# Optimization experiments

Measured on AMD Instinct MI355X. Metric: run time of the kernel, lower is better.

Reference implementation:

```python
import jax, jax.numpy as jnp
import numpy as np

SPLINE_ORDER = 3
TOP_K = 2
NUM_EXPERTS = 8


def _gram_basis(x, beta_w):
    # x: (B, C, H, W) post-tanh. Returns (B, C*(S+1), H, W).
    P0 = jnp.ones_like(x)
    P1 = x
    ps = [P0, P1]
    for i in range(2, SPLINE_ORDER + 1):
        n, m = i - 1, i
        # beta(n, m) = (m+n)*(m-n)*n^2 / (m^2/(4n^2-1)) * beta_weights[n]
        beta = (m + n) * (m - n) * (n ** 2) * (4.0 * n ** 2 - 1.0) / (m ** 2) * beta_w[n]
        P2 = x * ps[-1] - beta * ps[-2]
        ps.append(P2)
    return jnp.concatenate(ps, axis=1)


def _expert(x, poly_w, beta_w):
    # tanh -> Gram polynomial basis -> SiLU -> conv2d (padding=1, stride=1)
    g = jax.nn.silu(_gram_basis(jnp.tanh(x), beta_w))
    return jax.lax.conv_general_dilated(
        g, poly_w[0], window_strides=(1, 1), padding=[(1, 1), (1, 1)],
        dimension_numbers=('NCHW', 'OIHW', 'NCHW'))


def _cv_squared(v):
    # torch.var is unbiased (ddof=1)
    return jnp.var(v, ddof=1) / (jnp.mean(v) ** 2 + 1e-10)


def reference(x, w_gate, poly_weights, beta_weights):
    B = x.shape[0]
    # gating input: global average pool -> (B, C)
    gate_x = jnp.mean(x, axis=(2, 3))
    probs = jax.nn.softmax(gate_x @ w_gate, axis=1)  # softmax BEFORE topk, as in source
    top_vals, top_idx = jax.lax.top_k(probs, TOP_K + 1)
    tk_vals = top_vals[:, :TOP_K]
    tk_idx = top_idx[:, :TOP_K]
    tk_gates = tk_vals / (jnp.sum(tk_vals, axis=1, keepdims=True) + 1e-6)
    gates = jnp.zeros_like(probs).at[jnp.arange(B)[:, None], tk_idx].set(tk_gates)
    importance = gates.sum(axis=0)
    load = jnp.sum(gates > 0, axis=0).astype(jnp.float32)  # eval-mode load
    loss = (_cv_squared(importance) + _cv_squared(load)) * 0.01
    # All experts share parameters (ModuleList([experts]*num_experts)), so
    # sum_e gates[b,e] * expert_e(x[b]) == gates.sum(1)[b] * expert(x[b]).
    y = _expert(x, poly_weights, beta_weights) * jnp.sum(gates, axis=1)[:, None, None, None]
    return y, loss


def setup_inputs() -> dict:
    key = jax.random.key(0)
    k1, k2, k3, k4 = jax.random.split(key, 4)
    x = jax.random.normal(k1, (16, 32, 192, 192), dtype=jnp.float32)
    w_gate = jax.random.normal(k2, (32, NUM_EXPERTS), dtype=jnp.float32) * 0.1
    poly_weights = jax.random.normal(k3, (1, 32, 32 * (SPLINE_ORDER + 1), 3, 3), dtype=jnp.float32) * 0.05
    beta_weights = jax.random.normal(k4, (SPLINE_ORDER + 1,), dtype=jnp.float32) * 0.01
    return {"x": x, "w_gate": w_gate, "poly_weights": poly_weights, "beta_weights": beta_weights}
```

## Files before the change

### kernel.cpp

```cpp
#include <hip/hip_runtime.h>

typedef unsigned short u16;
typedef unsigned int u32;
typedef __attribute__((ext_vector_type(8))) short bf16x8;
typedef __attribute__((ext_vector_type(4))) float f32x4;

static constexpr int B = 16, C = 32, H = 192, W = 192;
static constexpr int HW = H * W;
static constexpr int E = 8;
static constexpr int CO = 32;
static constexpr int NB = 96;
static constexpr long long NTOT = (long long)B * C * HW;
static constexpr float SILU1 = 0.7310585786300049f;

static constexpr size_t GP_OFF  = (size_t)NTOT * 2;
static constexpr size_t SCL_OFF = GP_OFF + (size_t)B * C * NB * 4;
static constexpr size_t SK_OFF  = SCL_OFF + 128;
static constexpr size_t SS_OFF  = SK_OFF + 288 * 4;
static constexpr size_t WF_OFF  = SS_OFF + 128;

__device__ inline u32 cvt_pk_bf16(float lo, float hi) {
    u32 r;
    asm("v_cvt_pk_bf16_f32 %0, %1, %2" : "=v"(r) : "v"(lo), "v"(hi));
    return r;
}
__device__ inline u16 f2b(float f) {
    u32 u = __float_as_uint(f);
    return (u16)((u + 0x7fffu + ((u >> 16) & 1u)) >> 16);
}
__device__ inline float silu_fast(float z) {
    return z * __builtin_amdgcn_rcpf(1.0f + __expf(-z));
}
__device__ inline float tanh_fast(float z) {
    float e = __expf(2.0f * z);
    return 1.0f - 2.0f * __builtin_amdgcn_rcpf(e + 1.0f);
}

__global__ __launch_bounds__(256) void stage1_prep(const float* __restrict__ x,
                                                   const float* __restrict__ pw,
                                                   u16* __restrict__ t_out,
                                                   float* __restrict__ gpart,
                                                   float* __restrict__ Sk,
                                                   float* __restrict__ Ssum,
                                                   u16* __restrict__ wfrag) {
    __shared__ float sg[2][4][16];
    __shared__ float sred[9][32][8];
    __shared__ float sks[288];
    const int blk = blockIdx.x, tid = threadIdx.x;
    if (blk < B * NB) {
        const int b = blk / NB, band = blk - (blk / NB) * NB;
        const int cp = tid & 15, part = tid >> 4;
        const size_t pbase = (size_t)b * HW + (size_t)(band * 2) * W;
        const float4* xa = (const float4*)(x + (size_t)(b * C + 2 * cp) * HW
                                             + (size_t)(band * 2) * W);
        const float4* xb = (const float4*)(x + (size_t)(b * C + 2 * cp + 1) * HW
                                             + (size_t)(band * 2) * W);
        u32* tw = (u32*)t_out;
        float s0 = 0.0f, s1 = 0.0f;
        #pragma unroll
        for (int k = 0; k < 6; ++k) {
            const int j = k * 16 + part;
            float4 a = xa[j], c = xb[j];
            s0 += (a.x + a.y) + (a.z + a.w);
            s1 += (c.x + c.y) + (c.z + c.w);
            u32 r0 = cvt_pk_bf16(tanh_fast(a.x), tanh_fast(c.x));
            u32 r1 = cvt_pk_bf16(tanh_fast(a.y), tanh_fast(c.y));
            u32 r2 = cvt_pk_bf16(tanh_fast(a.z), tanh_fast(c.z));
            u32 r3 = cvt_pk_bf16(tanh_fast(a.w), tanh_fast(c.w));
            u32* dst = tw + (pbase + (size_t)j * 4) * 16 + cp;
            dst[0] = r0; dst[16] = r1; dst[32] = r2; dst[48] = r3;
        }
        s0 += __shfl_down(s0, 32); s0 += __shfl_down(s0, 16);
        s1 += __shfl_down(s1, 32); s1 += __shfl_down(s1, 16);
        if ((part & 3) == 0) { sg[0][tid >> 6][cp] = s0; sg[1][tid >> 6][cp] = s1; }
        __syncthreads();
        if (tid < 32) {
            const int cpp = tid >> 1, o = tid & 1;
            gpart[(size_t)(b * C + tid) * NB + band] =
                (sg[o][0][cpp] + sg[o][1][cpp]) + (sg[o][2][cpp] + sg[o][3][cpp]);
        }
        return;
    }
    if (blk < B * NB + 108) {
        int j = (blk - B * NB) * 256 + tid;
        int e = j & 7, lane = (j >> 3) & 63, rest = j >> 9;
        int half = rest & 1, pt = rest >> 1;
        int p = pt / 9, tap = pt - p * 9;
        int co = half * 16 + (lane & 15);
        int ci = 32 + p * 32 + (lane >> 4) * 8 + e;
        wfrag[j] = f2b(pw[(size_t)co * 1152 + ci * 9 + tap]);
        return;
    }
    {
        const int co = tid & 31, sub = tid >> 5;
        #pragma unroll
        for (int k = 0; k < 9; ++k) {
            float s = 0.0f;
            #pragma unroll
            for (int i = 0; i < 4; ++i)
                s += pw[(size_t)co * 1152 + (sub * 4 + i) * 9 + k];
            sred[k][co][sub] = s;
        }
        __syncthreads();
        for (int j = tid; j < 288; j += 256) {
            int k = j >> 5, c = j & 31;
            float s = 0.0f;
            #pragma unroll
            for (int u = 0; u < 8; ++u) s += sred[k][c][u];
            sks[j] = s; Sk[j] = s;
        }
        __syncthreads();
        if (tid < 32) {
            float s = 0.0f;
            #pragma unroll
            for (int k = 0; k < 9; ++k) s += sks[k * 32 + tid];
            Ssum[tid] = s;
        }
    }
}

__global__ __launch_bounds__(512) void gate_k(const float* __restrict__ gpart,
                                              const float* __restrict__ wg,
                                              float* __restrict__ scl,
                                              float* __restrict__ out) {
    __shared__ float gx[B][C];
    __shared__ float lg[B][E];
    __shared__ float gt[B][E];
    const int tid = threadIdx.x;
    {
        const float4* gp = (const float4*)(gpart + (size_t)tid * NB);
        float s = 0.0f;
        #pragma unroll
        for (int k = 0; k < NB / 4; ++k) { float4 v = gp[k]; s += (v.x + v.y) + (v.z + v.w); }
        gx[tid >> 5][tid & 31] = s * (1.0f / HW);
    }
    __syncthreads();
    if (tid < B * E) {
        const int gb = tid >> 3, ge = tid & 7;
        float s = 0.0f;
        #pragma unroll
        for (int c = 0; c < C; ++c) s += gx[gb][c] * wg[c * E + ge];
        lg[gb][ge] = s;
    }
    __syncthreads();
    if (tid < B) {
        float p[E];
        float m = lg[tid][0];
        #pragma unroll
        for (int e = 1; e < E; ++e) m = fmaxf(m, lg[tid][e]);
        float sum = 0.0f;
        #pragma unroll
        for (int e = 0; e < E; ++e) { p[e] = __expf(lg[tid][e] - m); sum += p[e]; }
        float inv = 1.0f / sum;
        #pragma unroll
        for (int e = 0; e < E; ++e) p[e] *= inv;
        int i0 = 0; float v0g = p[0];
        #pragma unroll
        for (int e = 1; e < E; ++e) if (p[e] > v0g) { v0g = p[e]; i0 = e; }
        int i1 = -1; float v1g = -1.0f;
        #pragma unroll
        for (int e = 0; e < E; ++e) { if (e == i0) continue; if (p[e] > v1g) { v1g = p[e]; i1 = e; } }
        const float denom = v0g + v1g + 1e-6f;
        #pragma unroll
        for (int e = 0; e < E; ++e) gt[tid][e] = 0.0f;
        gt[tid][i0] = v0g / denom; gt[tid][i1] = v1g / denom;
        scl[tid] = gt[tid][i0] + gt[tid][i1];
    }
    __syncthreads();
    if (tid == 0) {
        float imp[E], ld[E];
        #pragma unroll
        for (int e = 0; e < E; ++e) { imp[e] = 0.0f; ld[e] = 0.0f; }
        for (int bb = 0; bb < B; ++bb)
            #pragma unroll
            for (int e = 0; e < E; ++e) {
                float g = gt[bb][e];
                imp[e] += g;
                if (g > 0.0f) ld[e] += 1.0f;
            }
        float mi = 0.0f, mld = 0.0f;
        #pragma unroll
        for (int e = 0; e < E; ++e) { mi += imp[e]; mld += ld[e]; }
        mi *= (1.0f / E); mld *= (1.0f / E);
        float vi = 0.0f, vl = 0.0f;
        #pragma unroll
        for (int e = 0; e < E; ++e) {
            float di = imp[e] - mi, dl = ld[e] - mld;
            vi += di * di; vl += dl * dl;
        }
        vi *= (1.0f / (E - 1)); vl *= (1.0f / (E - 1));
        out[NTOT] = (vi / (mi * mi + 1e-10f) + vl / (mld * mld + 1e-10f)) * 0.01f;
    }
}

static constexpr int GSTR = 40;

__global__ __launch_bounds__(256, 3) void conv_mfma(const u16* __restrict__ t_ws,
                                                 const u16* __restrict__ wfrag,
                                                 const float* __restrict__ beta_w,
                                                 const float* __restrict__ scl_ws,
                                                 const float* __restrict__ Sk,
                                                 const float* __restrict__ Ssum,
                                                 float* __restrict__ out) {
    __shared__ __align__(16) u16 gtile[2][324 * GSTR];

    const int b = blockIdx.z;
    const int gx0 = blockIdx.x << 4, gy0 = blockIdx.y << 4;
    const int tid = threadIdx.x;
    const int w = tid >> 6, lane = tid & 63, q = lane >> 4, ml = lane & 15;
    const float beta2 = 2.25f * beta_w[1];
    const float beta23 = beta2 + (300.0f / 9.0f) * beta_w[2];

    const int p0 = tid;
    int extra = -1;
    if ((tid & 3) == 0) extra = tid >> 2;
    else if ((tid & 63) == 1) extra = 64 + (tid >> 6);
    const int p1 = (extra >= 0) ? 256 + extra : -1;

    u32 pk0[16], pk1[16];
    bool v0, v1 = false;
    {
        int py = p0 / 18, px = p0 - py * 18;
        int gy = gy0 + py - 1, gx = gx0 + px - 1;
        v0 = (unsigned)gy < (unsigned)H && (unsigned)gx < (unsigned)W;
        if (v0) {
            const uint4* tp = (const uint4*)(t_ws + (((size_t)b * HW + (size_t)gy * W + gx) << 5));
            *(uint4*)&pk0[0]  = tp[0];
            *(uint4*)&pk0[4]  = tp[1];
            *(uint4*)&pk0[8]  = tp[2];
            *(uint4*)&pk0[12] = tp[3];
        } else {
            #pragma unroll
            for (int cc = 0; cc < 16; ++cc) pk0[cc] = 0u;
        }
        if (p1 >= 0) {
            int py1 = p1 / 18, px1 = p1 - py1 * 18;
            int gy1 = gy0 + py1 - 1, gx1 = gx0 + px1 - 1;
            v1 = (unsigned)gy1 < (unsigned)H && (unsigned)gx1 < (unsigned)W;
            if (v1) {
                const uint4* tp = (const uint4*)(t_ws + (((size_t)b * HW + (size_t)gy1 * W + gx1) << 5));
                *(uint4*)&pk1[0]  = tp[0];
                *(uint4*)&pk1[4]  = tp[1];
                *(uint4*)&pk1[8]  = tp[2];
                *(uint4*)&pk1[12] = tp[3];
            }
        }
        if (!v1) {
            #pragma unroll
            for (int cc = 0; cc < 16; ++cc) pk1[cc] = 0u;
        }
    }

    const float sc = scl_ws[b];

#define BQUAD(P, BUF, SLOT, QI)                                                 \
    do {                                                                        \
        if (!(SLOT) || p1 >= 0) {                                               \
            const bool vv = (SLOT) ? v1 : v0;                                   \
            const u32* pk = (SLOT) ? pk1 : pk0;                                 \
            const int pix = (SLOT) ? p1 : p0;                                   \
            u32 rq[4];                                                          \
            if (vv) {                                                           \
                _Pragma("unroll")                                               \
                for (int i = 0; i < 4; ++i) {                                   \
                    const int cc = (QI) * 4 + i;                                \
                    float tl = __uint_as_float(pk[cc] << 16);                   \
                    float th = __uint_as_float(pk[cc] & 0xffff0000u);           \
                    float ul, uh;                                               \
                    if ((P) == 0) { ul = tl; uh = th; }                         \
                    else if ((P) == 1) { ul = fmaf(tl, tl, -beta2); uh = fmaf(th, th, -beta2); } \
                    else { ul = tl * fmaf(tl, tl, -beta23); uh = th * fmaf(th, th, -beta23); } \
                    rq[i] = cvt_pk_bf16(silu_fast(ul), silu_fast(uh));          \
                }                                                               \
            } else { rq[0] = 0u; rq[1] = 0u; rq[2] = 0u; rq[3] = 0u; }          \
            *(uint4*)&gtile[BUF][pix * GSTR + (QI) * 8] = *(const uint4*)rq;    \
        }                                                                       \
    } while (0)

    f32x4 acc[4][2];
    #pragma unroll
    for (int a = 0; a < 4; ++a) {
        acc[a][0] = (f32x4){0.0f, 0.0f, 0.0f, 0.0f};
        acc[a][1] = (f32x4){0.0f, 0.0f, 0.0f, 0.0f};
    }

#define MFMA_DX(P, BUF, DX, ...)                                                \
    do {                                                                        \
        const u16* wf = wfrag + (size_t)(P) * 9216;                             \
        bf16x8 bfr[3][2];                                                       \
        _Pragma("unroll")                                                       \
        for (int dyi = 0; dyi < 3; ++dyi) {                                     \
            const int tap = dyi * 3 + (DX);                                     \
            bfr[dyi][0] = *(const bf16x8*)(wf + ((size_t)(tap * 2 + 0) * 64 + lane) * 8); \
            bfr[dyi][1] = *(const bf16x8*)(wf + ((size_t)(tap * 2 + 1) * 64 + lane) * 8); \
        }                                                                       \
        bf16x8 af6[6];                                                          \
        _Pragma("unroll")                                                       \
        for (int rl = 0; rl < 6; ++rl)                                          \
            af6[rl] = *(const bf16x8*)                                          \
                &gtile[BUF][(((w << 2) + rl) * 18 + ml + (DX)) * GSTR + (q << 3)]; \
        __VA_ARGS__;                                                            \
        _Pragma("unroll")                                                       \
        for (int rl = 0; rl < 6; ++rl) {                                        \
            _Pragma("unroll")                                                   \
            for (int dyi = 0; dyi < 3; ++dyi) {                                 \
                const int a = rl - dyi;                                         \
                if (a >= 0 && a < 4) {                                          \
                    acc[a][0] = __builtin_amdgcn_mfma_f32_16x16x32_bf16(af6[rl], bfr[dyi][0], acc[a][0], 0, 0, 0); \
                    acc[a][1] = __builtin_amdgcn_mfma_f32_16x16x32_bf16(af6[rl], bfr[dyi][1], acc[a][1], 0, 0, 0); \
                }                                                               \
            }                                                                   \
        }                                                                       \
    } while (0)

    BQUAD(0, 0, 0, 0); BQUAD(0, 0, 0, 1); BQUAD(0, 0, 0, 2); BQUAD(0, 0, 0, 3);
    BQUAD(0, 0, 1, 0); BQUAD(0, 0, 1, 1); BQUAD(0, 0, 1, 2); BQUAD(0, 0, 1, 3);
    __syncthreads();
    MFMA_DX(0, 0, 0, BQUAD(1, 1, 0, 0); BQUAD(1, 1, 0, 1); BQUAD(1, 1, 0, 2));
    MFMA_DX(0, 0, 1, BQUAD(1, 1, 0, 3); BQUAD(1, 1, 1, 0); BQUAD(1, 1, 1, 1));
    MFMA_DX(0, 0, 2, BQUAD(1, 1, 1, 2); BQUAD(1, 1, 1, 3));
    __syncthreads();
    MFMA_DX(1, 1, 0, BQUAD(2, 0, 0, 0); BQUAD(2, 0, 0, 1); BQUAD(2, 0, 0, 2));
    MFMA_DX(1, 1, 1, BQUAD(2, 0, 0, 3); BQUAD(2, 0, 1, 0); BQUAD(2, 0, 1, 1));
    MFMA_DX(1, 1, 2, BQUAD(2, 0, 1, 2); BQUAD(2, 0, 1, 3));
    __syncthreads();
    MFMA_DX(2, 0, 0, (void)0);
    MFMA_DX(2, 0, 1, (void)0);
    MFMA_DX(2, 0, 2, (void)0);

#undef BQUAD
#undef MFMA_DX

    const bool interior = (blockIdx.x > 0) && (blockIdx.x < 11) &&
                          (blockIdx.y > 0) && (blockIdx.y < 11);
    #pragma unroll
    for (int half = 0; half < 2; ++half) {
        const int co = half * 16 + ml;
        const float bfull = SILU1 * Ssum[co];
        #pragma unroll
        for (int a = 0; a < 4; ++a) {
            const int y = gy0 + (w << 2) + a;
            float ov[4];
            #pragma unroll
            for (int r = 0; r < 4; ++r) {
                float bias = bfull;
                if (!interior) {
                    const int xg = gx0 + (q << 2) + r;
                    bias = 0.0f;
                    #pragma unroll
                    for (int k = 0; k < 9; ++k) {
                        int yy = y + k / 3 - 1, xx = xg + k % 3 - 1;
                        if ((unsigned)yy < (unsigned)H && (unsigned)xx < (unsigned)W)
                            bias += Sk[k * 32 + co];
                    }
                    bias *= SILU1;
                }
                ov[r] = (acc[a][half][r] + bias) * sc;
            }
            *(float4*)&out[((size_t)(b * CO + co) * H + y) * W + gx0 + (q << 2)] = *(float4*)ov;
        }
    }
}

extern "C" void kernel_launch(void* const* d_in, const int* in_sizes, int n_in,
                              void* d_out, int out_size, void* d_ws, size_t ws_size,
                              hipStream_t stream) {
    const float* x  = (const float*)d_in[0];
    const float* wg = (const float*)d_in[1];
    const float* pw = (const float*)d_in[2];
    const float* bw = (const float*)d_in[3];
    float* out = (float*)d_out;
    char* ws = (char*)d_ws;
    u16*   t_ws  = (u16*)ws;
    float* gpart = (float*)(ws + GP_OFF);
    float* scl   = (float*)(ws + SCL_OFF);
    float* Sk    = (float*)(ws + SK_OFF);
    float* Ssum  = (float*)(ws + SS_OFF);
    u16*   wfrag = (u16*)(ws + WF_OFF);

    stage1_prep<<<dim3(B * NB + 109), 256, 0, stream>>>(x, pw, t_ws, gpart, Sk, Ssum, wfrag);
    gate_k<<<dim3(1), 512, 0, stream>>>(gpart, wg, scl, out);
    conv_mfma<<<dim3(12, 12, B), 256, 0, stream>>>(t_ws, wfrag, bw, scl, Sk, Ssum, out);
}
```

Measured before the change: 242.2 us.

## Fuse gating into prep kernel, stage tanh via LDS, single-buffer conv tile

The separate gate kernel is folded into stage1_prep: the last band block, found with an atomic counter, computes the softmax, top-k gates and loss. Stage1 now transposes the bf16 tanh values through an LDS tile and writes coalesced 64-byte pixel rows instead of strided 32-bit stores. The conv kernel drops its double-buffered basis tile in favour of one buffer with sequential basis/MFMA phases, and raises launch bounds to 6 blocks per CU for more occupancy. This gives up the overlap of basis computation with MFMA and adds a memset and atomic serialization.

```diff
diff --git a/kernel.cpp b/kernel.cpp
--- a/kernel.cpp
+++ b/kernel.cpp
@@ -18,6 +18,7 @@
 static constexpr size_t SK_OFF  = SCL_OFF + 128;
 static constexpr size_t SS_OFF  = SK_OFF + 288 * 4;
 static constexpr size_t WF_OFF  = SS_OFF + 128;
+static constexpr size_t CNT_OFF = WF_OFF + 27648 * 2;
 
 __device__ inline u32 cvt_pk_bf16(float lo, float hi) {
     u32 r;
@@ -36,48 +37,133 @@
     return 1.0f - 2.0f * __builtin_amdgcn_rcpf(e + 1.0f);
 }
 
+static constexpr int TBS = 40;
+
 __global__ __launch_bounds__(256) void stage1_prep(const float* __restrict__ x,
                                                    const float* __restrict__ pw,
+                                                   const float* __restrict__ wg,
                                                    u16* __restrict__ t_out,
                                                    float* __restrict__ gpart,
                                                    float* __restrict__ Sk,
                                                    float* __restrict__ Ssum,
-                                                   u16* __restrict__ wfrag) {
-    __shared__ float sg[2][4][16];
-    __shared__ float sred[9][32][8];
-    __shared__ float sks[288];
+                                                   u16* __restrict__ wfrag,
+                                                   float* __restrict__ scl,
+                                                   u32* __restrict__ cnt,
+                                                   float* __restrict__ out) {
+    __shared__ __align__(16) char smem[384 * TBS * 2];
+    __shared__ u32 lastflag;
     const int blk = blockIdx.x, tid = threadIdx.x;
     if (blk < B * NB) {
         const int b = blk / NB, band = blk - (blk / NB) * NB;
-        const int cp = tid & 15, part = tid >> 4;
+        const int c = tid >> 3, s = tid & 7;
+        u16* tb = (u16*)smem;
+        const float4* xp = (const float4*)(x + (size_t)(b * C + c) * HW
+                                             + (size_t)(band * 2) * W);
+        float gsum = 0.0f;
+        #pragma unroll
+        for (int it = 0; it < 12; ++it) {
+            const int j = it * 8 + s;
+            float4 v = xp[j];
+            gsum += (v.x + v.y) + (v.z + v.w);
+            const int px = j * 4;
+            tb[(px + 0) * TBS + c] = f2b(tanh_fast(v.x));
+            tb[(px + 1) * TBS + c] = f2b(tanh_fast(v.y));
+            tb[(px + 2) * TBS + c] = f2b(tanh_fast(v.z));
+            tb[(px + 3) * TBS + c] = f2b(tanh_fast(v.w));
+        }
+        gsum += __shfl_down(gsum, 4, 8);
+        gsum += __shfl_down(gsum, 2, 8);
+        gsum += __shfl_down(gsum, 1, 8);
+        if (s == 0) gpart[(size_t)(b * C + c) * NB + band] = gsum;
+        __syncthreads();
         const size_t pbase = (size_t)b * HW + (size_t)(band * 2) * W;
-        const float4* xa = (const float4*)(x + (size_t)(b * C + 2 * cp) * HW
-                                             + (size_t)(band * 2) * W);
-        const float4* xb = (const float4*)(x + (size_t)(b * C + 2 * cp + 1) * HW
-                                             + (size_t)(band * 2) * W);
-        u32* tw = (u32*)t_out;
-        float s0 = 0.0f, s1 = 0.0f;
-        #pragma unroll
-        for (int k = 0; k < 6; ++k) {
-            const int j = k * 16 + part;
-            float4 a = xa[j], c = xb[j];
-            s0 += (a.x + a.y) + (a.z + a.w);
-            s1 += (c.x + c.y) + (c.z + c.w);
-            u32 r0 = cvt_pk_bf16(tanh_fast(a.x), tanh_fast(c.x));
-            u32 r1 = cvt_pk_bf16(tanh_fast(a.y), tanh_fast(c.y));
-            u32 r2 = cvt_pk_bf16(tanh_fast(a.z), tanh_fast(c.z));
-            u32 r3 = cvt_pk_bf16(tanh_fast(a.w), tanh_fast(c.w));
-            u32* dst = tw + (pbase + (size_t)j * 4) * 16 + cp;
-            dst[0] = r0; dst[16] = r1; dst[32] = r2; dst[48] = r3;
-        }
-        s0 += __shfl_down(s0, 32); s0 += __shfl_down(s0, 16);
-        s1 += __shfl_down(s1, 32); s1 += __shfl_down(s1, 16);
-        if ((part & 3) == 0) { sg[0][tid >> 6][cp] = s0; sg[1][tid >> 6][cp] = s1; }
-        __syncthreads();
-        if (tid < 32) {
-            const int cpp = tid >> 1, o = tid & 1;
-            gpart[(size_t)(b * C + tid) * NB + band] =
-                (sg[o][0][cpp] + sg[o][1][cpp]) + (sg[o][2][cpp] + sg[o][3][cpp]);
+        uint4* tw = (uint4*)t_out;
+        {
+            const uint4* row = (const uint4*)(tb + tid * TBS);
+            uint4* dst = tw + (pbase + tid) * 4;
+            dst[0] = row[0]; dst[1] = row[1]; dst[2] = row[2]; dst[3] = row[3];
+        }
+        if (tid < 128) {
+            const int p = 256 + tid;
+            const uint4* row = (const uint4*)(tb + p * TBS);
+            uint4* dst = tw + (pbase + p) * 4;
+            dst[0] = row[0]; dst[1] = row[1]; dst[2] = row[2]; dst[3] = row[3];
+        }
+        __threadfence();
+        __syncthreads();
+        if (tid == 0) {
+            u32 tk = atomicAdd(cnt, 1u);
+            __threadfence();
+            lastflag = (tk == (u32)(B * NB - 1)) ? 1u : 0u;
+        }
+        __syncthreads();
+        if (!lastflag) return;
+        float* gxs = (float*)smem;
+        float* lgs = gxs + 512;
+        float* gts = lgs + 128;
+        for (int r = tid; r < B * C; r += 256) {
+            const float4* gp = (const float4*)(gpart + (size_t)r * NB);
+            float ss = 0.0f;
+            #pragma unroll
+            for (int k = 0; k < NB / 4; ++k) { float4 v = gp[k]; ss += (v.x + v.y) + (v.z + v.w); }
+            gxs[r] = ss * (1.0f / HW);
+        }
+        __syncthreads();
+        if (tid < B * E) {
+            const int gb = tid >> 3, ge = tid & 7;
+            float ssum = 0.0f;
+            #pragma unroll
+            for (int cc = 0; cc < C; ++cc) ssum += gxs[gb * 32 + cc] * wg[cc * E + ge];
+            lgs[tid] = ssum;
+        }
+        __syncthreads();
+        if (tid < B) {
+            float p[E];
+            float m = lgs[tid * E];
+            #pragma unroll
+            for (int e = 1; e < E; ++e) m = fmaxf(m, lgs[tid * E + e]);
+            float sum = 0.0f;
+            #pragma unroll
+            for (int e = 0; e < E; ++e) { p[e] = __expf(lgs[tid * E + e] - m); sum += p[e]; }
+            float inv = 1.0f / sum;
+            #pragma unroll
+            for (int e = 0; e < E; ++e) p[e] *= inv;
+            int i0 = 0; float v0g = p[0];
+            #pragma unroll
+            for (int e = 1; e < E; ++e) if (p[e] > v0g) { v0g = p[e]; i0 = e; }
+            int i1 = -1; float v1g = -1.0f;
+            #pragma unroll
+            for (int e = 0; e < E; ++e) { if (e == i0) continue; if (p[e] > v1g) { v1g = p[e]; i1 = e; } }
+            const float denom = v0g + v1g + 1e-6f;
+            #pragma unroll
+            for (int e = 0; e < E; ++e) gts[tid * E + e] = 0.0f;
+            gts[tid * E + i0] = v0g / denom; gts[tid * E + i1] = v1g / denom;
+            scl[tid] = gts[tid * E + i0] + gts[tid * E + i1];
+        }
+        __syncthreads();
+        if (tid == 0) {
+            float imp[E], ld[E];
+            #pragma unroll
+            for (int e = 0; e < E; ++e) { imp[e] = 0.0f; ld[e] = 0.0f; }
+            for (int bb = 0; bb < B; ++bb)
+                #pragma unroll
+                for (int e = 0; e < E; ++e) {
+                    float g = gts[bb * E + e];
+                    imp[e] += g;
+                    if (g > 0.0f) ld[e] += 1.0f;
+                }
+            float mi = 0.0f, mld = 0.0f;
+            #pragma unroll
+            for (int e = 0; e < E; ++e) { mi += imp[e]; mld += ld[e]; }
+            mi *= (1.0f / E); mld *= (1.0f / E);
+            float vi = 0.0f, vl = 0.0f;
+            #pragma unroll
+            for (int e = 0; e < E; ++e) {
+                float di = imp[e] - mi, dl = ld[e] - mld;
+                vi += di * di; vl += dl * dl;
+            }
+            vi *= (1.0f / (E - 1)); vl *= (1.0f / (E - 1));
+            out[NTOT] = (vi / (mi * mi + 1e-10f) + vl / (mld * mld + 1e-10f)) * 0.01f;
         }
         return;
     }
@@ -92,6 +178,8 @@
         return;
     }
     {
+        float* sred = (float*)smem;
+        float* sks  = (float*)(smem + 9216);
         const int co = tid & 31, sub = tid >> 5;
         #pragma unroll
         for (int k = 0; k < 9; ++k) {
@@ -99,14 +187,13 @@
             #pragma unroll
             for (int i = 0; i < 4; ++i)
                 s += pw[(size_t)co * 1152 + (sub * 4 + i) * 9 + k];
-            sred[k][co][sub] = s;
+            sred[(k * 32 + co) * 8 + sub] = s;
         }
         __syncthreads();
         for (int j = tid; j < 288; j += 256) {
-            int k = j >> 5, c = j & 31;
             float s = 0.0f;
             #pragma unroll
-            for (int u = 0; u < 8; ++u) s += sred[k][c][u];
+            for (int u = 0; u < 8; ++u) s += sred[j * 8 + u];
             sks[j] = s; Sk[j] = s;
         }
         __syncthreads();
@@ -119,90 +206,16 @@
     }
 }
 
-__global__ __launch_bounds__(512) void gate_k(const float* __restrict__ gpart,
-                                              const float* __restrict__ wg,
-                                              float* __restrict__ scl,
-                                              float* __restrict__ out) {
-    __shared__ float gx[B][C];
-    __shared__ float lg[B][E];
-    __shared__ float gt[B][E];
-    const int tid = threadIdx.x;
-    {
-        const float4* gp = (const float4*)(gpart + (size_t)tid * NB);
-        float s = 0.0f;
-        #pragma unroll
-        for (int k = 0; k < NB / 4; ++k) { float4 v = gp[k]; s += (v.x + v.y) + (v.z + v.w); }
-        gx[tid >> 5][tid & 31] = s * (1.0f / HW);
-    }
-    __syncthreads();
-    if (tid < B * E) {
-        const int gb = tid >> 3, ge = tid & 7;
-        float s = 0.0f;
-        #pragma unroll
-        for (int c = 0; c < C; ++c) s += gx[gb][c] * wg[c * E + ge];
-        lg[gb][ge] = s;
-    }
-    __syncthreads();
-    if (tid < B) {
-        float p[E];
-        float m = lg[tid][0];
-        #pragma unroll
-        for (int e = 1; e < E; ++e) m = fmaxf(m, lg[tid][e]);
-        float sum = 0.0f;
-        #pragma unroll
-        for (int e = 0; e < E; ++e) { p[e] = __expf(lg[tid][e] - m); sum += p[e]; }
-        float inv = 1.0f / sum;
-        #pragma unroll
-        for (int e = 0; e < E; ++e) p[e] *= inv;
-        int i0 = 0; float v0g = p[0];
-        #pragma unroll
-        for (int e = 1; e < E; ++e) if (p[e] > v0g) { v0g = p[e]; i0 = e; }
-        int i1 = -1; float v1g = -1.0f;
-        #pragma unroll
-        for (int e = 0; e < E; ++e) { if (e == i0) continue; if (p[e] > v1g) { v1g = p[e]; i1 = e; } }
-        const float denom = v0g + v1g + 1e-6f;
-        #pragma unroll
-        for (int e = 0; e < E; ++e) gt[tid][e] = 0.0f;
-        gt[tid][i0] = v0g / denom; gt[tid][i1] = v1g / denom;
-        scl[tid] = gt[tid][i0] + gt[tid][i1];
-    }
-    __syncthreads();
-    if (tid == 0) {
-        float imp[E], ld[E];
-        #pragma unroll
-        for (int e = 0; e < E; ++e) { imp[e] = 0.0f; ld[e] = 0.0f; }
-        for (int bb = 0; bb < B; ++bb)
-            #pragma unroll
-            for (int e = 0; e < E; ++e) {
-                float g = gt[bb][e];
-                imp[e] += g;
-                if (g > 0.0f) ld[e] += 1.0f;
-            }
-        float mi = 0.0f, mld = 0.0f;
-        #pragma unroll
-        for (int e = 0; e < E; ++e) { mi += imp[e]; mld += ld[e]; }
-        mi *= (1.0f / E); mld *= (1.0f / E);
-        float vi = 0.0f, vl = 0.0f;
-        #pragma unroll
-        for (int e = 0; e < E; ++e) {
-            float di = imp[e] - mi, dl = ld[e] - mld;
-            vi += di * di; vl += dl * dl;
-        }
-        vi *= (1.0f / (E - 1)); vl *= (1.0f / (E - 1));
-        out[NTOT] = (vi / (mi * mi + 1e-10f) + vl / (mld * mld + 1e-10f)) * 0.01f;
-    }
-}
-
 static constexpr int GSTR = 40;
 
-__global__ __launch_bounds__(256, 3) void conv_mfma(const u16* __restrict__ t_ws,
+__global__ __launch_bounds__(256, 6) void conv_mfma(const u16* __restrict__ t_ws,
                                                  const u16* __restrict__ wfrag,
                                                  const float* __restrict__ beta_w,
                                                  const float* __restrict__ scl_ws,
                                                  const float* __restrict__ Sk,
                                                  const float* __restrict__ Ssum,
                                                  float* __restrict__ out) {
-    __shared__ __align__(16) u16 gtile[2][324 * GSTR];
+    __shared__ __align__(16) u16 gtile[324 * GSTR];
 
     const int b = blockIdx.z;
     const int gx0 = blockIdx.x << 4, gy0 = blockIdx.y << 4;
@@ -253,27 +266,35 @@
 
     const float sc = scl_ws[b];
 
-#define BQUAD(P, BUF, SLOT, QI)                                                 \
+#define BASIS(P)                                                                \
     do {                                                                        \
-        if (!(SLOT) || p1 >= 0) {                                               \
-            const bool vv = (SLOT) ? v1 : v0;                                   \
-            const u32* pk = (SLOT) ? pk1 : pk0;                                 \
-            const int pix = (SLOT) ? p1 : p0;                                   \
-            u32 rq[4];                                                          \
+        _Pragma("unroll")                                                       \
+        for (int slot = 0; slot < 2; ++slot) {                                  \
+            const int pix = slot ? p1 : p0;                                     \
+            if (slot && p1 < 0) continue;                                       \
+            const bool vv = slot ? v1 : v0;                                     \
+            const u32* pk = slot ? pk1 : pk0;                                   \
+            u32 r[16];                                                          \
             if (vv) {                                                           \
                 _Pragma("unroll")                                               \
-                for (int i = 0; i < 4; ++i) {                                   \
-                    const int cc = (QI) * 4 + i;                                \
+                for (int cc = 0; cc < 16; ++cc) {                               \
                     float tl = __uint_as_float(pk[cc] << 16);                   \
                     float th = __uint_as_float(pk[cc] & 0xffff0000u);           \
                     float ul, uh;                                               \
                     if ((P) == 0) { ul = tl; uh = th; }                         \
                     else if ((P) == 1) { ul = fmaf(tl, tl, -beta2); uh = fmaf(th, th, -beta2); } \
                     else { ul = tl * fmaf(tl, tl, -beta23); uh = th * fmaf(th, th, -beta23); } \
-                    rq[i] = cvt_pk_bf16(silu_fast(ul), silu_fast(uh));          \
+                    r[cc] = cvt_pk_bf16(silu_fast(ul), silu_fast(uh));          \
                 }                                                               \
-            } else { rq[0] = 0u; rq[1] = 0u; rq[2] = 0u; rq[3] = 0u; }          \
-            *(uint4*)&gtile[BUF][pix * GSTR + (QI) * 8] = *(const uint4*)rq;    \
+            } else {                                                            \
+                _Pragma("unroll")                                               \
+                for (int cc = 0; cc < 16; ++cc) r[cc] = 0u;                     \
+            }                                                                   \
+            uint4* dst = (uint4*)&gtile[pix * GSTR];                            \
+            dst[0] = *(const uint4*)&r[0];                                      \
+            dst[1] = *(const uint4*)&r[4];                                      \
+            dst[2] = *(const uint4*)&r[8];                                      \
+            dst[3] = *(const uint4*)&r[12];                                     \
         }                                                                       \
     } while (0)
 
@@ -284,7 +305,7 @@
         acc[a][1] = (f32x4){0.0f, 0.0f, 0.0f, 0.0f};
     }
 
-#define MFMA_DX(P, BUF, DX, ...)                                                \
+#define MFMA_DX(P, DX)                                                          \
     do {                                                                        \
         const u16* wf = wfrag + (size_t)(P) * 9216;                             \
         bf16x8 bfr[3][2];                                                       \
@@ -298,8 +319,7 @@
         _Pragma("unroll")                                                       \
         for (int rl = 0; rl < 6; ++rl)                                          \
             af6[rl] = *(const bf16x8*)                                          \
-                &gtile[BUF][(((w << 2) + rl) * 18 + ml + (DX)) * GSTR + (q << 3)]; \
-        __VA_ARGS__;                                                            \
+                &gtile[(((w << 2) + rl) * 18 + ml + (DX)) * GSTR + (q << 3)];   \
         _Pragma("unroll")                                                       \
         for (int rl = 0; rl < 6; ++rl) {                                        \
             _Pragma("unroll")                                                   \
@@ -313,22 +333,19 @@
         }                                                                       \
     } while (0)
 
-    BQUAD(0, 0, 0, 0); BQUAD(0, 0, 0, 1); BQUAD(0, 0, 0, 2); BQUAD(0, 0, 0, 3);
-    BQUAD(0, 0, 1, 0); BQUAD(0, 0, 1, 1); BQUAD(0, 0, 1, 2); BQUAD(0, 0, 1, 3);
+    BASIS(0);
     __syncthreads();
-    MFMA_DX(0, 0, 0, BQUAD(1, 1, 0, 0); BQUAD(1, 1, 0, 1); BQUAD(1, 1, 0, 2));
-    MFMA_DX(0, 0, 1, BQUAD(1, 1, 0, 3); BQUAD(1, 1, 1, 0); BQUAD(1, 1, 1, 1));
-    MFMA_DX(0, 0, 2, BQUAD(1, 1, 1, 2); BQUAD(1, 1, 1, 3));
+    MFMA_DX(0, 0); MFMA_DX(0, 1); MFMA_DX(0, 2);
     __syncthreads();
-    MFMA_DX(1, 1, 0, BQUAD(2, 0, 0, 0); BQUAD(2, 0, 0, 1); BQUAD(2, 0, 0, 2));
-    MFMA_DX(1, 1, 1, BQUAD(2, 0, 0, 3); BQUAD(2, 0, 1, 0); BQUAD(2, 0, 1, 1));
-    MFMA_DX(1, 1, 2, BQUAD(2, 0, 1, 2); BQUAD(2, 0, 1, 3));
+    BASIS(1);
     __syncthreads();
-    MFMA_DX(2, 0, 0, (void)0);
-    MFMA_DX(2, 0, 1, (void)0);
-    MFMA_DX(2, 0, 2, (void)0);
-
-#undef BQUAD
+    MFMA_DX(1, 0); MFMA_DX(1, 1); MFMA_DX(1, 2);
+    __syncthreads();
+    BASIS(2);
+    __syncthreads();
+    MFMA_DX(2, 0); MFMA_DX(2, 1); MFMA_DX(2, 2);
+
+#undef BASIS
 #undef MFMA_DX
 
     const bool interior = (blockIdx.x > 0) && (blockIdx.x < 11) &&
@@ -377,8 +394,10 @@
     float* Sk    = (float*)(ws + SK_OFF);
     float* Ssum  = (float*)(ws + SS_OFF);
     u16*   wfrag = (u16*)(ws + WF_OFF);
-
-    stage1_prep<<<dim3(B * NB + 109), 256, 0, stream>>>(x, pw, t_ws, gpart, Sk, Ssum, wfrag);
-    gate_k<<<dim3(1), 512, 0, stream>>>(gpart, wg, scl, out);
+    u32*   cnt   = (u32*)(ws + CNT_OFF);
+
+    hipMemsetAsync(cnt, 0, 4, stream);
+    stage1_prep<<<dim3(B * NB + 109), 256, 0, stream>>>(x, pw, wg, t_ws, gpart,
+                                                        Sk, Ssum, wfrag, scl, cnt, out);
     conv_mfma<<<dim3(12, 12, B), 256, 0, stream>>>(t_ws, wfrag, bw, scl, Sk, Ssum, out);
 }
```

New measurement: 674.2 us. 178% more time.
